# Optimization experiments

Measured on AMD Instinct MI355X. Metric: run time of the kernel, lower is better.

Reference implementation:

```python
import jax, jax.numpy as jnp
import numpy as np

INF = 1000000000000000.0  # 1e15, matches the TF source

B, H, S, D = 4, 16, 1024, 64


def setup_inputs() -> dict:
    key = jax.random.key(0)
    kq, kk, kv, kp = jax.random.split(key, 4)
    q = jax.random.normal(kq, (B, H, S, D), dtype=jnp.float32)
    k = jax.random.normal(kk, (B, H, S, D), dtype=jnp.float32)
    v = jax.random.normal(kv, (B, H, S, D), dtype=jnp.float32)
    # pad_mask: 1 = masked-out key position, broadcast over heads and queries
    pad_mask = jax.random.randint(kp, (B, 1, 1, S), 0, 2, dtype=jnp.int32)
    # look_ahead_mask: 1 above the diagonal (future positions masked)
    look_ahead_mask = jnp.triu(jnp.ones((S, S), dtype=jnp.int32), k=1)[None, None]
    return {"q": q, "k": k, "v": v, "pad_mask": pad_mask,
            "look_ahead_mask": look_ahead_mask}


def reference(q, k, v, pad_mask, look_ahead_mask):
    d_model = jnp.float32(q.shape[3])
    # scores: (B, H, Sq, Sk)
    score_logits = jnp.einsum("bhqd,bhkd->bhqk", q, k) / jnp.sqrt(d_model)
    if pad_mask is not None:
        score_logits = score_logits + pad_mask.astype(jnp.float32) * (-INF)
    if look_ahead_mask is not None:
        score_logits = score_logits + look_ahead_mask.astype(jnp.float32) * (-INF)
    attention_weights = jax.nn.softmax(score_logits, axis=-1)
    context_vector = jnp.einsum("bhqk,bhkd->bhqd", attention_weights, v)
    return (context_vector, attention_weights)
```

## Files before the change

### kernel.cpp

```cpp
#include <hip/hip_runtime.h>
#include <stdint.h>

#define S 1024
#define D 64
#define TQ 16
#define KT 128
#define NKT 8
#define NEG (-1e15f)
#define SCALE 0.125f

#define WB_STRIDE 1048
#define KB_STRIDE 72
#define VT_STRIDE 136
#define QS_STRIDE 72

typedef __bf16 bf16x8 __attribute__((ext_vector_type(8)));
typedef float f32x4 __attribute__((ext_vector_type(4)));
typedef unsigned short ushort_t;

__device__ __forceinline__ unsigned short f2b(float f) {
  union { float f; uint32_t u; } c; c.f = f;
  uint32_t u = c.u;
  return (unsigned short)((u + 0x7fffu + ((u >> 16) & 1u)) >> 16);
}
__device__ __forceinline__ float b2f(uint32_t u) {
  union { uint32_t u; float f; } c; c.u = u << 16;
  return c.f;
}

__global__ __launch_bounds__(256) void prep_k_kernel(
    const float* __restrict__ Kg, ushort_t* __restrict__ Kb)
{
  const size_t idx = ((size_t)blockIdx.x * 256 + threadIdx.x) * 8;
  float4 a = *(const float4*)(Kg + idx);
  float4 b = *(const float4*)(Kg + idx + 4);
  ushort_t tmp[8];
  tmp[0]=f2b(a.x); tmp[1]=f2b(a.y); tmp[2]=f2b(a.z); tmp[3]=f2b(a.w);
  tmp[4]=f2b(b.x); tmp[5]=f2b(b.y); tmp[6]=f2b(b.z); tmp[7]=f2b(b.w);
  *(uint4*)(Kb + idx) = *(const uint4*)tmp;
}

__global__ __launch_bounds__(256) void prep_vt_kernel(
    const float* __restrict__ Vg, ushort_t* __restrict__ Vt)
{
  __shared__ __align__(16) ushort_t lvt[D * QS_STRIDE];
  const int t = threadIdx.x;
  const int bh = blockIdx.x >> 4;
  const int j0 = (blockIdx.x & 15) << 6;

  {
    const int j = t >> 2, sd = (t & 3) << 4;
    const float* src = Vg + ((size_t)bh * S + j0 + j) * D + sd;
#pragma unroll
    for (int c = 0; c < 4; ++c) {
      float4 f = *(const float4*)(src + (c << 2));
      lvt[(sd + (c << 2) + 0) * QS_STRIDE + j] = f2b(f.x);
      lvt[(sd + (c << 2) + 1) * QS_STRIDE + j] = f2b(f.y);
      lvt[(sd + (c << 2) + 2) * QS_STRIDE + j] = f2b(f.z);
      lvt[(sd + (c << 2) + 3) * QS_STRIDE + j] = f2b(f.w);
    }
  }
  __syncthreads();
  {
    const int d = t >> 2, sj = (t & 3) << 4;
    ushort_t tmp[16];
#pragma unroll
    for (int c = 0; c < 4; ++c)
      *(ushort4*)&tmp[c << 2] = *(const ushort4*)&lvt[d * QS_STRIDE + sj + (c << 2)];
    ushort_t* dst = Vt + ((size_t)bh * D + d) * S + j0 + sj;
    *(uint4*)dst = *(const uint4*)&tmp[0];
    *(uint4*)(dst + 8) = *(const uint4*)&tmp[8];
  }
}

__global__ __launch_bounds__(512, 6) void attn_kernel(
    const float* __restrict__ Qg, const ushort_t* __restrict__ Kb,
    const ushort_t* __restrict__ Vtb, const int* __restrict__ PADg,
    float* __restrict__ OCTX, float* __restrict__ OW)
{
  __shared__ __align__(16) ushort_t wb[TQ * WB_STRIDE];
  __shared__ __align__(16) ushort_t ub[KT * KB_STRIDE];

  const int t  = threadIdx.x;
  const int w  = t >> 6;
  const int l  = t & 63;
  const int la = l & 15;
  const int lb = l >> 4;
  const int blk = blockIdx.x;
  const int bh  = blk >> 6;
  const int qt  = blk & 63;
  const int qr0 = qt << 4;

  const size_t head = (size_t)bh * S * D;
  const int* pp = PADg + (size_t)(bh >> 4) * S;

  bf16x8 aq0, aq1;
  {
    const float* qrow = Qg + head + (size_t)(qr0 + la) * D + (lb << 3);
    float4 q00 = *(const float4*)(qrow);
    float4 q01 = *(const float4*)(qrow + 4);
    float4 q10 = *(const float4*)(qrow + 32);
    float4 q11 = *(const float4*)(qrow + 36);
    ushort_t a0[8], a1[8];
    a0[0]=f2b(q00.x); a0[1]=f2b(q00.y); a0[2]=f2b(q00.z); a0[3]=f2b(q00.w);
    a0[4]=f2b(q01.x); a0[5]=f2b(q01.y); a0[6]=f2b(q01.z); a0[7]=f2b(q01.w);
    a1[0]=f2b(q10.x); a1[1]=f2b(q10.y); a1[2]=f2b(q10.z); a1[3]=f2b(q10.w);
    a1[4]=f2b(q11.x); a1[5]=f2b(q11.y); a1[6]=f2b(q11.z); a1[7]=f2b(q11.w);
    aq0 = *(const bf16x8*)a0;
    aq1 = *(const bf16x8*)a1;
  }

  for (int kt = 0; kt < NKT; ++kt) {
    {
      const ushort_t* kp = Kb + head + (size_t)(kt * KT) * D;
      const int row = t >> 2, off = (t & 3) << 4;
      const ushort_t* src = kp + row * D + off;
      ushort_t* dst = &ub[row * KB_STRIDE + off];
      *(uint4*)dst = *(const uint4*)src;
      *(uint4*)(dst + 8) = *(const uint4*)(src + 8);
    }
    __syncthreads();
    {
      const int j0 = w << 4;
      f32x4 acc = {0.f, 0.f, 0.f, 0.f};
      bf16x8 b0 = *(const bf16x8*)&ub[(j0 + la) * KB_STRIDE + (lb << 3)];
      acc = __builtin_amdgcn_mfma_f32_16x16x32_bf16(aq0, b0, acc, 0, 0, 0);
      bf16x8 b1 = *(const bf16x8*)&ub[(j0 + la) * KB_STRIDE + 32 + (lb << 3)];
      acc = __builtin_amdgcn_mfma_f32_16x16x32_bf16(aq1, b1, acc, 0, 0, 0);
#pragma unroll
      for (int i = 0; i < 4; ++i)
        wb[((lb << 2) + i) * WB_STRIDE + kt * KT + j0 + la] = f2b(acc[i]);
    }
    __syncthreads();
  }

#pragma unroll
  for (int rr = 0; rr < 2; ++rr) {
    const int r  = (w << 1) + rr;
    const int qr = qr0 + r;
    float lg[16];
    float m = -3.0e38f;
#pragma unroll
    for (int ii = 0; ii < 8; ++ii) {
      const int j = (l << 1) + (ii << 7);
      uint32_t pr = *(const uint32_t*)&wb[r * WB_STRIDE + j];
      int2 pv = *(const int2*)&pp[j];
      float l0 = b2f(pr & 0xffffu) * SCALE + (pv.x ? NEG : 0.0f) + ((j     > qr) ? NEG : 0.0f);
      float l1 = b2f(pr >> 16)     * SCALE + (pv.y ? NEG : 0.0f) + ((j + 1 > qr) ? NEG : 0.0f);
      lg[2 * ii] = l0; lg[2 * ii + 1] = l1;
      m = fmaxf(m, fmaxf(l0, l1));
    }
#pragma unroll
    for (int off = 32; off > 0; off >>= 1) m = fmaxf(m, __shfl_xor(m, off, 64));
    float sum = 0.f;
#pragma unroll
    for (int x = 0; x < 16; ++x) { lg[x] = __expf(lg[x] - m); sum += lg[x]; }
#pragma unroll
    for (int off = 32; off > 0; off >>= 1) sum += __shfl_xor(sum, off, 64);
    const float inv = 1.0f / sum;
    float* orow = OW + (size_t)(bh * S + qr) * S;
#pragma unroll
    for (int ii = 0; ii < 8; ++ii) {
      const int j = (l << 1) + (ii << 7);
      float w0 = lg[2 * ii] * inv, w1 = lg[2 * ii + 1] * inv;
      *(uint32_t*)&wb[r * WB_STRIDE + j] = ((uint32_t)f2b(w1) << 16) | (uint32_t)f2b(w0);
      *(float2*)&orow[j] = make_float2(w0, w1);
    }
  }
  __syncthreads();

  const int jh = w >> 2;
  const int d0 = (w & 3) << 4;
  f32x4 cacc = {0.f, 0.f, 0.f, 0.f};
  for (int kt = 0; kt < NKT; ++kt) {
    {
      const ushort_t* vp = Vtb + (size_t)bh * D * S + kt * KT;
      const int dd = t >> 3, off = (t & 7) << 4;
      const ushort_t* src = vp + (size_t)dd * S + off;
      ushort_t* dst = &ub[dd * VT_STRIDE + off];
      *(uint4*)dst = *(const uint4*)src;
      *(uint4*)(dst + 8) = *(const uint4*)(src + 8);
    }
    __syncthreads();
#pragma unroll
    for (int ks = 0; ks < 2; ++ks) {
      const int jt = jh * 64 + ks * 32;
      bf16x8 af = *(const bf16x8*)&wb[la * WB_STRIDE + kt * KT + jt + (lb << 3)];
      bf16x8 bf = *(const bf16x8*)&ub[(d0 + la) * VT_STRIDE + jt + (lb << 3)];
      cacc = __builtin_amdgcn_mfma_f32_16x16x32_bf16(af, bf, cacc, 0, 0, 0);
    }
    __syncthreads();
  }

  float* pbuf = (float*)ub;
  if (w >= 4) {
#pragma unroll
    for (int i = 0; i < 4; ++i)
      pbuf[(w - 4) * 320 + ((lb << 2) + i) * 20 + la] = cacc[i];
  }
  __syncthreads();
  if (w < 4) {
#pragma unroll
    for (int i = 0; i < 4; ++i) {
      const int qrow = (lb << 2) + i;
      OCTX[((size_t)(bh * S) + qr0 + qrow) * D + d0 + la] =
          cacc[i] + pbuf[w * 320 + qrow * 20 + la];
    }
  }
}

extern "C" void kernel_launch(void* const* d_in, const int* in_sizes, int n_in,
                              void* d_out, int out_size, void* d_ws, size_t ws_size,
                              hipStream_t stream) {
  const float* q   = (const float*)d_in[0];
  const float* k   = (const float*)d_in[1];
  const float* v   = (const float*)d_in[2];
  const int*   pad = (const int*)d_in[3];
  float* ctx  = (float*)d_out;
  float* wout = (float*)d_out + (size_t)4 * 16 * S * D;

  ushort_t* Kb  = (ushort_t*)d_ws;
  ushort_t* Vtb = (ushort_t*)d_ws + (size_t)4 * 16 * S * D;

  prep_k_kernel <<<dim3(2048), dim3(256), 0, stream>>>(k, Kb);
  prep_vt_kernel<<<dim3(1024), dim3(256), 0, stream>>>(v, Vtb);
  attn_kernel   <<<dim3(4096), dim3(512), 0, stream>>>(q, Kb, Vtb, pad, ctx, wout);
}
```

Measured before the change: 409.4 us.

## Load K and V^T fragments directly from global memory and use nontemporal output stores

Removes the shared-memory staging buffer for K and V^T tiles, so each wave reads its MFMA operands straight from global memory (through L2/L1). This drops the per-tile __syncthreads barriers and the LDS round trip, frees LDS for higher occupancy, and reuses the weight buffer for the final partial-sum reduction. Output stores for the attention weights and the context switch to nontemporal to avoid polluting the cache. The cost is uncoalesced, partly redundant global loads for K and V, because several waves read the same rows.

Result: slower. 437.9 us (+7.0%).

```diff
diff --git a/kernel.cpp b/kernel.cpp
--- a/kernel.cpp
+++ b/kernel.cpp
@@ -10,8 +10,6 @@
 #define SCALE 0.125f
 
 #define WB_STRIDE 1048
-#define KB_STRIDE 72
-#define VT_STRIDE 136
 #define QS_STRIDE 72
 
 typedef __bf16 bf16x8 __attribute__((ext_vector_type(8)));
@@ -79,7 +77,6 @@
     float* __restrict__ OCTX, float* __restrict__ OW)
 {
   __shared__ __align__(16) ushort_t wb[TQ * WB_STRIDE];
-  __shared__ __align__(16) ushort_t ub[KT * KB_STRIDE];
 
   const int t  = threadIdx.x;
   const int w  = t >> 6;
@@ -110,29 +107,22 @@
     aq1 = *(const bf16x8*)a1;
   }
 
-  for (int kt = 0; kt < NKT; ++kt) {
-    {
-      const ushort_t* kp = Kb + head + (size_t)(kt * KT) * D;
-      const int row = t >> 2, off = (t & 3) << 4;
-      const ushort_t* src = kp + row * D + off;
-      ushort_t* dst = &ub[row * KB_STRIDE + off];
-      *(uint4*)dst = *(const uint4*)src;
-      *(uint4*)(dst + 8) = *(const uint4*)(src + 8);
-    }
-    __syncthreads();
-    {
-      const int j0 = w << 4;
+  {
+    const ushort_t* kcol = Kb + head + (size_t)((w << 4) + la) * D + (lb << 3);
+#pragma unroll
+    for (int kt = 0; kt < NKT; ++kt) {
+      const ushort_t* kr = kcol + (size_t)(kt * KT) * D;
       f32x4 acc = {0.f, 0.f, 0.f, 0.f};
-      bf16x8 b0 = *(const bf16x8*)&ub[(j0 + la) * KB_STRIDE + (lb << 3)];
+      bf16x8 b0 = *(const bf16x8*)(kr);
       acc = __builtin_amdgcn_mfma_f32_16x16x32_bf16(aq0, b0, acc, 0, 0, 0);
-      bf16x8 b1 = *(const bf16x8*)&ub[(j0 + la) * KB_STRIDE + 32 + (lb << 3)];
+      bf16x8 b1 = *(const bf16x8*)(kr + 32);
       acc = __builtin_amdgcn_mfma_f32_16x16x32_bf16(aq1, b1, acc, 0, 0, 0);
 #pragma unroll
       for (int i = 0; i < 4; ++i)
-        wb[((lb << 2) + i) * WB_STRIDE + kt * KT + j0 + la] = f2b(acc[i]);
-    }
-    __syncthreads();
-  }
+        wb[((lb << 2) + i) * WB_STRIDE + kt * KT + (w << 4) + la] = f2b(acc[i]);
+    }
+  }
+  __syncthreads();
 
 #pragma unroll
   for (int rr = 0; rr < 2; ++rr) {
@@ -164,7 +154,9 @@
       const int j = (l << 1) + (ii << 7);
       float w0 = lg[2 * ii] * inv, w1 = lg[2 * ii + 1] * inv;
       *(uint32_t*)&wb[r * WB_STRIDE + j] = ((uint32_t)f2b(w1) << 16) | (uint32_t)f2b(w0);
-      *(float2*)&orow[j] = make_float2(w0, w1);
+      unsigned long long uw = ((unsigned long long)__float_as_uint(w1) << 32)
+                            | (unsigned long long)__float_as_uint(w0);
+      __builtin_nontemporal_store(uw, (unsigned long long*)&orow[j]);
     }
   }
   __syncthreads();
@@ -172,27 +164,23 @@
   const int jh = w >> 2;
   const int d0 = (w & 3) << 4;
   f32x4 cacc = {0.f, 0.f, 0.f, 0.f};
-  for (int kt = 0; kt < NKT; ++kt) {
-    {
-      const ushort_t* vp = Vtb + (size_t)bh * D * S + kt * KT;
-      const int dd = t >> 3, off = (t & 7) << 4;
-      const ushort_t* src = vp + (size_t)dd * S + off;
-      ushort_t* dst = &ub[dd * VT_STRIDE + off];
-      *(uint4*)dst = *(const uint4*)src;
-      *(uint4*)(dst + 8) = *(const uint4*)(src + 8);
-    }
-    __syncthreads();
-#pragma unroll
-    for (int ks = 0; ks < 2; ++ks) {
-      const int jt = jh * 64 + ks * 32;
-      bf16x8 af = *(const bf16x8*)&wb[la * WB_STRIDE + kt * KT + jt + (lb << 3)];
-      bf16x8 bf = *(const bf16x8*)&ub[(d0 + la) * VT_STRIDE + jt + (lb << 3)];
-      cacc = __builtin_amdgcn_mfma_f32_16x16x32_bf16(af, bf, cacc, 0, 0, 0);
-    }
-    __syncthreads();
-  }
-
-  float* pbuf = (float*)ub;
+  {
+    const ushort_t* vrow = Vtb + (size_t)bh * D * S + (size_t)(d0 + la) * S
+                          + jh * 64 + (lb << 3);
+#pragma unroll
+    for (int kt = 0; kt < NKT; ++kt) {
+#pragma unroll
+      for (int ks = 0; ks < 2; ++ks) {
+        const int jt = jh * 64 + ks * 32;
+        bf16x8 af = *(const bf16x8*)&wb[la * WB_STRIDE + kt * KT + jt + (lb << 3)];
+        bf16x8 bf = *(const bf16x8*)(vrow + kt * KT + ks * 32);
+        cacc = __builtin_amdgcn_mfma_f32_16x16x32_bf16(af, bf, cacc, 0, 0, 0);
+      }
+    }
+  }
+  __syncthreads();
+
+  float* pbuf = (float*)wb;
   if (w >= 4) {
 #pragma unroll
     for (int i = 0; i < 4; ++i)
@@ -203,8 +191,9 @@
 #pragma unroll
     for (int i = 0; i < 4; ++i) {
       const int qrow = (lb << 2) + i;
-      OCTX[((size_t)(bh * S) + qr0 + qrow) * D + d0 + la] =
-          cacc[i] + pbuf[w * 320 + qrow * 20 + la];
+      __builtin_nontemporal_store(
+          cacc[i] + pbuf[w * 320 + qrow * 20 + la],
+          &OCTX[((size_t)(bh * S) + qr0 + qrow) * D + d0 + la]);
     }
   }
 }
```
